# Kernel tuning notes

Measured on AMD Instinct MI355X. Metric: run time of the kernel, lower is better.

The kernel has to match this reference:

```python
import jax, jax.numpy as jnp
import numpy as np

B, C, N = 8, 64, 4096

def setup_inputs() -> dict:
    key = jax.random.key(0)
    k1, k2, k3 = jax.random.split(key, 3)
    k = jax.random.normal(k1, (B, C, N), dtype=jnp.float32)
    q = jax.random.normal(k2, (B, C, N), dtype=jnp.float32)
    v = jax.random.normal(k3, (B, C, N), dtype=jnpp.float32) if False else jax.random.normal(k3, (B, C, N), dtype=jnp.float32)
    return {"k": k, "q": q, "v": v}

def reference(k, q, v):
    input_dim = k.shape[1]  # C
    # similarity = k^T @ q : [B, N, N]
    scores = jnp.einsum('bcn,bcm->bnm', k, q) / jnp.sqrt(jnp.float32(input_dim))
    attn = jax.nn.softmax(scores, axis=-1)  # softmax over last dim (query positions m)
    # out = attn @ v^T : [B, N, C], then transpose back to [B, C, N]
    out = jnp.einsum('bnm,bcm->bcn', attn, v)
    return out
```

## Files before the change

kernel.cpp:

```cpp
#include <hip/hip_runtime.h>
#include <stdint.h>

typedef __attribute__((ext_vector_type(8)))  __bf16        bf16x8;
typedef __attribute__((ext_vector_type(8)))  unsigned short u16x8;
typedef __attribute__((ext_vector_type(4)))  float          f32x4;
typedef __attribute__((ext_vector_type(16))) float          f32x16;
typedef __attribute__((ext_vector_type(4)))  unsigned int   u32x4;

#define NB 8
#define NC 64
#define NN 4096
#define NCHUNK 64
#define CHUNK_U16 4096

#define EXP2F(x) __builtin_amdgcn_exp2f(x)

__device__ __forceinline__ unsigned short f2bf(float x) {
    unsigned int u = __builtin_bit_cast(unsigned int, x);
    u += 0x7fffu + ((u >> 16) & 1u);
    return (unsigned short)(u >> 16);
}
__device__ __forceinline__ unsigned int pk2(float a, float b) {
    unsigned short x = __builtin_bit_cast(unsigned short, (__bf16)a);
    unsigned short y = __builtin_bit_cast(unsigned short, (__bf16)b);
    return (unsigned int)x | ((unsigned int)y << 16);
}

__global__ __launch_bounds__(256) void prepass(
    const float* __restrict__ qp, const float* __restrict__ vp,
    unsigned short* __restrict__ qfo, unsigned short* __restrict__ vfo)
{
    __shared__ float lt[64][68];
    const int bid = blockIdx.x;
    const int b = bid >> 6, mc = bid & 63;
    const int m0 = mc * 64;
    const int tid = threadIdx.x;
    const float* qb = qp + (size_t)b * NC * NN;
    const float* vb = vp + (size_t)b * NC * NN;
    unsigned short* qfc = qfo + (size_t)bid * CHUNK_U16;
    unsigned short* vfc = vfo + (size_t)bid * CHUNK_U16;

    #pragma unroll
    for (int rep = 0; rep < 4; ++rep) {
        int idx = tid + 256 * rep;
        int c = idx >> 4, m4 = (idx & 15) << 2;
        f32x4 xv = *reinterpret_cast<const f32x4*>(qb + (size_t)c * NN + m0 + m4);
        lt[m4+0][c] = xv[0]; lt[m4+1][c] = xv[1];
        lt[m4+2][c] = xv[2]; lt[m4+3][c] = xv[3];
    }
    __syncthreads();
    #pragma unroll
    for (int rep = 0; rep < 2; ++rep) {
        int fid = tid + 256 * rep;
        int l = fid & 63, kk = (fid >> 6) & 3, mt = fid >> 8;
        int m = 32 * mt + (l & 31), c0 = 16 * kk + 8 * (l >> 5);
        u16x8 ov;
        #pragma unroll
        for (int e = 0; e < 8; ++e) ov[e] = f2bf(lt[m][c0 + e]);
        *reinterpret_cast<u16x8*>(qfc + (size_t)fid * 8) = ov;
    }
    __syncthreads();
    #pragma unroll
    for (int rep = 0; rep < 4; ++rep) {
        int idx = tid + 256 * rep;
        int c = idx >> 4, m4 = (idx & 15) << 2;
        f32x4 xv = *reinterpret_cast<const f32x4*>(vb + (size_t)c * NN + m0 + m4);
        *reinterpret_cast<f32x4*>(&lt[c][m4]) = xv;
    }
    __syncthreads();
    #pragma unroll
    for (int rep = 0; rep < 2; ++rep) {
        int fid = tid + 256 * rep;
        int l = fid & 63, kt = (fid >> 6) & 3, ct = fid >> 8;
        int c = 32 * ct + (l & 31), mm = 16 * kt + 8 * (l >> 5);
        u16x8 ov;
        #pragma unroll
        for (int e = 0; e < 8; ++e) ov[e] = f2bf(lt[c][mm + e]);
        *reinterpret_cast<u16x8*>(vfc + (size_t)fid * 8) = ov;
    }
}

template<int SPLITQ_T>
__global__ __launch_bounds__(128, 3) void attn4(
    const float* __restrict__ kp,
    const unsigned short* __restrict__ qfo,
    const unsigned short* __restrict__ vfo,
    float* __restrict__ part, float* __restrict__ lp)
{
    constexpr int CPQ_T = NCHUNK / SPLITQ_T;
    __shared__ unsigned short sq[2][CHUNK_U16];

    const int orig = blockIdx.x;
    constexpr int PER_XCD = 64 * SPLITQ_T;
    const int bid = (orig & 7) * PER_XCD + (orig >> 3);
    const int b = bid / PER_XCD;
    const int rest = bid % PER_XCD;
    const int tile = rest & 63;
    const int qid  = rest >> 6;
    const int n0 = tile * 64;
    const int tid = threadIdx.x;
    const int w = tid >> 6, l = tid & 63;
    const int lo5 = l & 31, hi = l >> 5;
    const int nrow = n0 + 32 * w + lo5;

    const float kscale = 0.125f * 1.44269504088896f;
    const float* kb = kp + (size_t)b * NC * NN;
    bf16x8 kf[4];
    #pragma unroll
    for (int kk = 0; kk < 4; ++kk) {
        u16x8 t;
        #pragma unroll
        for (int e = 0; e < 8; ++e)
            t[e] = __builtin_bit_cast(unsigned short,
                      (__bf16)(kscale * kb[(size_t)(16 * kk + 8 * hi + e) * NN + nrow]));
        kf[kk] = __builtin_bit_cast(bf16x8, t);
    }

    const unsigned short* qg = qfo + (size_t)(b * NCHUNK + qid * CPQ_T) * CHUNK_U16;
    const unsigned short* vg = vfo + (size_t)(b * NCHUNK + qid * CPQ_T) * CHUNK_U16;

    auto stage_q = [&](int mcr, int buf) {
        const unsigned short* gq = qg + (size_t)mcr * CHUNK_U16;
        #pragma unroll
        for (int i = 0; i < 4; ++i) {
            int seg = w * 4 + i;
            int off = seg * 512 + l * 8;
            __builtin_amdgcn_global_load_lds(
                (const __attribute__((address_space(1))) void*)(gq + off),
                (__attribute__((address_space(3))) void*)(&sq[buf][seg * 512]),
                16, 0, 0);
        }
    };

    stage_q(0, 0);
    __syncthreads();

    f32x16 o0, o1;
    #pragma unroll
    for (int r = 0; r < 16; ++r) { o0[r] = 0.f; o1[r] = 0.f; }
    float l_run = 0.f;

    for (int mcr = 0; mcr < CPQ_T; ++mcr) {
        const int cur = mcr & 1;
        u16x8 vf[8];
        #pragma unroll
        for (int f = 0; f < 8; ++f)
            vf[f] = *reinterpret_cast<const u16x8*>(vg + (size_t)mcr * CHUNK_U16 + (f * 64 + l) * 8);
        if (mcr + 1 < CPQ_T) stage_q(mcr + 1, cur ^ 1);
        const unsigned short* qb_ = &sq[cur][0];

        f32x16 s0, s1;
        #pragma unroll
        for (int r = 0; r < 16; ++r) { s0[r] = 0.f; s1[r] = 0.f; }
        #pragma unroll
        for (int kk = 0; kk < 4; ++kk) {
            u16x8 a0 = *reinterpret_cast<const u16x8*>(qb_ + ((0 * 4 + kk) * 64 + l) * 8);
            u16x8 a1 = *reinterpret_cast<const u16x8*>(qb_ + ((1 * 4 + kk) * 64 + l) * 8);
            s0 = __builtin_amdgcn_mfma_f32_32x32x16_bf16(__builtin_bit_cast(bf16x8, a0), kf[kk], s0, 0, 0, 0);
            s1 = __builtin_amdgcn_mfma_f32_32x32x16_bf16(__builtin_bit_cast(bf16x8, a1), kf[kk], s1, 0, 0, 0);
        }

        float sum = 0.f;
        #pragma unroll
        for (int r = 0; r < 16; ++r) { s0[r] = EXP2F(s0[r]); sum += s0[r]; }
        #pragma unroll
        for (int r = 0; r < 16; ++r) { s1[r] = EXP2F(s1[r]); sum += s1[r]; }
        sum += (float)__shfl_xor(sum, 32);
        l_run += sum;

        #pragma unroll
        for (int kt = 0; kt < 4; ++kt) {
            const f32x16& sm = (kt < 2) ? s0 : s1;
            const int qA = 2 * (kt & 1);
            unsigned int wA0 = pk2(sm[4 * qA + 0], sm[4 * qA + 1]);
            unsigned int wA1 = pk2(sm[4 * qA + 2], sm[4 * qA + 3]);
            unsigned int wB0 = pk2(sm[4 * qA + 4], sm[4 * qA + 5]);
            unsigned int wB1 = pk2(sm[4 * qA + 6], sm[4 * qA + 7]);
            unsigned int e0 = hi ? wA0 : wB0;
            unsigned int e1 = hi ? wA1 : wB1;
            e0 = (unsigned int)__shfl_xor((int)e0, 32);
            e1 = (unsigned int)__shfl_xor((int)e1, 32);
            u32x4 pf;
            if (hi == 0) pf = (u32x4){wA0, wA1, e0, e1};
            else         pf = (u32x4){e0, e1, wB0, wB1};
            bf16x8 pB = __builtin_bit_cast(bf16x8, pf);
            o0 = __builtin_amdgcn_mfma_f32_32x32x16_bf16(__builtin_bit_cast(bf16x8, vf[kt]),     pB, o0, 0, 0, 0);
            o1 = __builtin_amdgcn_mfma_f32_32x32x16_bf16(__builtin_bit_cast(bf16x8, vf[4 + kt]), pB, o1, 0, 0, 0);
        }
        __syncthreads();
    }

    const int pidx = (b * 64 + tile) * SPLITQ_T + qid;
    float* po = part + (size_t)pidx * 4096;
    const int rl = 32 * w + lo5;
    #pragma unroll
    for (int r = 0; r < 16; ++r) {
        int cb = (r & 3) + 8 * (r >> 2) + 4 * hi;
        po[cb * 64 + rl]        = o0[r];
        po[(32 + cb) * 64 + rl] = o1[r];
    }
    if (hi == 0) lp[(size_t)pidx * 64 + rl] = l_run;
}

__global__ __launch_bounds__(256) void combine2(
    const float* __restrict__ part, const float* __restrict__ lp,
    float* __restrict__ outp, int splitq)
{
    __shared__ float sinv[64];
    const int bid = blockIdx.x;
    const int b = bid >> 6, tile = bid & 63;
    const int n0 = tile * 64;
    const int t = threadIdx.x;
    const int pb = bid * splitq;

    if (t < 64) {
        float L = 0.f;
        for (int q = 0; q < splitq; ++q) L += lp[(size_t)(pb + q) * 64 + t];
        sinv[t] = 1.0f / L;
    }
    __syncthreads();

    float* ob = outp + (size_t)b * NC * NN;
    #pragma unroll
    for (int it = 0; it < 4; ++it) {
        int idx = it * 1024 + t * 4;
        int ch = idx >> 6, r0 = idx & 63;
        f32x4 acc = (f32x4){0.f, 0.f, 0.f, 0.f};
        for (int q = 0; q < splitq; ++q) {
            f32x4 v = *reinterpret_cast<const f32x4*>(part + (size_t)(pb + q) * 4096 + idx);
            acc += v;
        }
        f32x4 res;
        #pragma unroll
        for (int u = 0; u < 4; ++u) res[u] = acc[u] * sinv[r0 + u];
        *reinterpret_cast<f32x4*>(ob + (size_t)ch * NN + n0 + r0) = res;
    }
}

__global__ __launch_bounds__(128) void attn2(
    const float* __restrict__ kp,
    const unsigned short* __restrict__ qfo,
    const unsigned short* __restrict__ vfo,
    float* __restrict__ outp)
{
    __shared__ unsigned short sb[2][2 * CHUNK_U16];
    const int orig = blockIdx.x;
    const int bid  = (orig & 7) * 64 + (orig >> 3);
    const int b = bid >> 6, nt = bid & 63;
    const int n0 = nt * 64;
    const int tid = threadIdx.x;
    const int w = tid >> 6, l = tid & 63;
    const int lo5 = l & 31, hi = l >> 5;
    const int nrow = n0 + 32 * w + lo5;
    const float kscale = 0.125f * 1.44269504088896f;
    const float* kb = kp + (size_t)b * NC * NN;
    bf16x8 kf[4];
    #pragma unroll
    for (int kk = 0; kk < 4; ++kk) {
        u16x8 t;
        #pragma unroll
        for (int e = 0; e < 8; ++e)
            t[e] = f2bf(kscale * kb[(size_t)(16 * kk + 8 * hi + e) * NN + nrow]);
        kf[kk] = __builtin_bit_cast(bf16x8, t);
    }
    const unsigned short* qg = qfo + (size_t)(b * 64) * CHUNK_U16;
    const unsigned short* vg = vfo + (size_t)(b * 64) * CHUNK_U16;
    auto stage = [&](int mc, int buf) {
        const unsigned short* gq = qg + (size_t)mc * CHUNK_U16;
        const unsigned short* gv = vg + (size_t)mc * CHUNK_U16;
        #pragma unroll
        for (int i = 0; i < 4; ++i) {
            int seg = w * 4 + i;
            int off = seg * 512 + l * 8;
            __builtin_amdgcn_global_load_lds(
                (const __attribute__((address_space(1))) void*)(gq + off),
                (__attribute__((address_space(3))) void*)(&sb[buf][seg * 512]), 16, 0, 0);
            __builtin_amdgcn_global_load_lds(
                (const __attribute__((address_space(1))) void*)(gv + off),
                (__attribute__((address_space(3))) void*)(&sb[buf][CHUNK_U16 + seg * 512]), 16, 0, 0);
        }
    };
    stage(0, 0);
    __syncthreads();
    f32x16 o0, o1;
    #pragma unroll
    for (int r = 0; r < 16; ++r) { o0[r] = 0.f; o1[r] = 0.f; }
    float m_run = -1e30f, l_run = 0.f;
    for (int mc = 0; mc < NCHUNK; ++mc) {
        const int cur = mc & 1;
        if (mc + 1 < NCHUNK) stage(mc + 1, cur ^ 1);
        const unsigned short* qb_ = &sb[cur][0];
        const unsigned short* vb_ = &sb[cur][CHUNK_U16];
        f32x16 s0, s1;
        #pragma unroll
        for (int r = 0; r < 16; ++r) { s0[r] = 0.f; s1[r] = 0.f; }
        #pragma unroll
        for (int kk = 0; kk < 4; ++kk) {
            u16x8 a0 = *reinterpret_cast<const u16x8*>(qb_ + ((0 * 4 + kk) * 64 + l) * 8);
            u16x8 a1 = *reinterpret_cast<const u16x8*>(qb_ + ((1 * 4 + kk) * 64 + l) * 8);
            s0 = __builtin_amdgcn_mfma_f32_32x32x16_bf16(__builtin_bit_cast(bf16x8, a0), kf[kk], s0, 0, 0, 0);
            s1 = __builtin_amdgcn_mfma_f32_32x32x16_bf16(__builtin_bit_cast(bf16x8, a1), kf[kk], s1, 0, 0, 0);
        }
        float pmax = s0[0];
        #pragma unroll
        for (int r = 1; r < 16; ++r) pmax = fmaxf(pmax, s0[r]);
        #pragma unroll
        for (int r = 0; r < 16; ++r) pmax = fmaxf(pmax, s1[r]);
        pmax = fmaxf(pmax, (float)__shfl_xor(pmax, 32));
        const float mn = fmaxf(m_run, pmax);
        const float alpha = EXP2F(m_run - mn);
        float sum = 0.f;
        #pragma unroll
        for (int r = 0; r < 16; ++r) { s0[r] = EXP2F(s0[r] - mn); sum += s0[r]; }
        #pragma unroll
        for (int r = 0; r < 16; ++r) { s1[r] = EXP2F(s1[r] - mn); sum += s1[r]; }
        sum += (float)__shfl_xor(sum, 32);
        l_run = l_run * alpha + sum;
        m_run = mn;
        #pragma unroll
        for (int r = 0; r < 16; ++r) { o0[r] *= alpha; o1[r] *= alpha; }
        #pragma unroll
        for (int kt = 0; kt < 4; ++kt) {
            const f32x16& sm = (kt < 2) ? s0 : s1;
            const int qA = 2 * (kt & 1);
            unsigned int dA0 = pk2(sm[4 * qA + 0], sm[4 * qA + 1]);
            unsigned int dA1 = pk2(sm[4 * qA + 2], sm[4 * qA + 3]);
            unsigned int dB0 = pk2(sm[4 * qA + 4], sm[4 * qA + 5]);
            unsigned int dB1 = pk2(sm[4 * qA + 6], sm[4 * qA + 7]);
            unsigned int sA0 = (unsigned int)__shfl_xor((int)dA0, 32);
            unsigned int sA1 = (unsigned int)__shfl_xor((int)dA1, 32);
            unsigned int sB0 = (unsigned int)__shfl_xor((int)dB0, 32);
            unsigned int sB1 = (unsigned int)__shfl_xor((int)dB1, 32);
            u32x4 pf;
            if (hi == 0) pf = (u32x4){dA0, dA1, sA0, sA1};
            else         pf = (u32x4){sB0, sB1, dB0, dB1};
            bf16x8 pB = __builtin_bit_cast(bf16x8, pf);
            u16x8 v0 = *reinterpret_cast<const u16x8*>(vb_ + ((0 * 4 + kt) * 64 + l) * 8);
            u16x8 v1 = *reinterpret_cast<const u16x8*>(vb_ + ((1 * 4 + kt) * 64 + l) * 8);
            o0 = __builtin_amdgcn_mfma_f32_32x32x16_bf16(__builtin_bit_cast(bf16x8, v0), pB, o0, 0, 0, 0);
            o1 = __builtin_amdgcn_mfma_f32_32x32x16_bf16(__builtin_bit_cast(bf16x8, v1), pB, o1, 0, 0, 0);
        }
        __syncthreads();
    }
    const float inv = 1.0f / l_run;
    float* ob = outp + (size_t)b * NC * NN;
    #pragma unroll
    for (int r = 0; r < 16; ++r) {
        int cb = (r & 3) + 8 * (r >> 2) + 4 * hi;
        ob[(size_t)cb * NN + n0 + 32 * w + lo5]        = o0[r] * inv;
        ob[(size_t)(32 + cb) * NN + n0 + 32 * w + lo5] = o1[r] * inv;
    }
}

__global__ __launch_bounds__(256) void attn_fwd(
    const float* __restrict__ kp, const float* __restrict__ qp,
    const float* __restrict__ vp, float* __restrict__ outp)
{
    __shared__ unsigned short qs[8][64][8];
    __shared__ unsigned short vs[8][64][8];
    __shared__ unsigned short ps[4][2][64][8];
    const int orig = blockIdx.x;
    const int bid  = (orig & 7) * 64 + (orig >> 3);
    const int b  = bid >> 6;
    const int n0 = (bid & 63) * 64;
    const int tid = threadIdx.x;
    const int w = tid >> 6, l = tid & 63, g = l >> 4, j = l & 15;
    const float* kb = kp + (size_t)b * NC * NN;
    const float* qb = qp + (size_t)b * NC * NN;
    const float* vb = vp + (size_t)b * NC * NN;
    bf16x8 ak[2];
    #pragma unroll
    for (int kk = 0; kk < 2; ++kk) {
        u16x8 tmp;
        #pragma unroll
        for (int e = 0; e < 8; ++e)
            tmp[e] = f2bf(kb[(size_t)(32*kk + 8*g + e) * NN + (n0 + 16*w + j)]);
        ak[kk] = __builtin_bit_cast(bf16x8, tmp);
    }
    f32x4 o[4];
    float m_run[4], l_run[4];
    #pragma unroll
    for (int ct = 0; ct < 4; ++ct) o[ct] = (f32x4){0.f,0.f,0.f,0.f};
    #pragma unroll
    for (int r = 0; r < 4; ++r) { m_run[r] = -1e30f; l_run[r] = 0.0f; }
    for (int m0 = 0; m0 < NN; m0 += 64) {
        __syncthreads();
        #pragma unroll
        for (int it = 0; it < 4; ++it) {
            int f = tid + 256*it;
            int c = f >> 4, m4 = (f & 15) << 2;
            f32x4 qv = *reinterpret_cast<const f32x4*>(qb + (size_t)c*NN + m0 + m4);
            f32x4 vv = *reinterpret_cast<const f32x4*>(vb + (size_t)c*NN + m0 + m4);
            int kkq = c >> 5, eq = c & 7, gq = (c >> 3) & 3, tq = m4 >> 4;
            #pragma unroll
            for (int u = 0; u < 4; ++u)
                qs[kkq*4 + tq][16*gq + ((m4 + u) & 15)][eq] = f2bf(qv[u]);
            int ctv = c >> 4, jv = c & 15, kkv = m4 >> 5, gv = (m4 >> 3) & 3, ev = m4 & 7;
            #pragma unroll
            for (int u = 0; u < 4; ++u)
                vs[kkv*4 + ctv][16*gv + jv][ev + u] = f2bf(vv[u]);
        }
        __syncthreads();
        f32x4 s[4];
        #pragma unroll
        for (int t = 0; t < 4; ++t) {
            f32x4 acc = (f32x4){0.f,0.f,0.f,0.f};
            #pragma unroll
            for (int kk = 0; kk < 2; ++kk) {
                u16x8 raw = *reinterpret_cast<const u16x8*>(&qs[kk*4 + t][l][0]);
                acc = __builtin_amdgcn_mfma_f32_16x16x32_bf16(ak[kk], __builtin_bit_cast(bf16x8, raw), acc, 0,0,0);
            }
            s[t] = acc * 0.125f;
        }
        float alpha[4];
        #pragma unroll
        for (int r = 0; r < 4; ++r) {
            float m1 = fmaxf(fmaxf(s[0][r], s[1][r]), fmaxf(s[2][r], s[3][r]));
            #pragma unroll
            for (int off = 1; off < 16; off <<= 1) m1 = fmaxf(m1, __shfl_xor(m1, off));
            float mn = fmaxf(m_run[r], m1);
            alpha[r] = __expf(m_run[r] - mn);
            m_run[r] = mn;
            float acc = 0.0f;
            #pragma unroll
            for (int t = 0; t < 4; ++t) { float p = __expf(s[t][r] - mn); s[t][r] = p; acc += p; }
            #pragma unroll
            for (int off = 1; off < 16; off <<= 1) acc += __shfl_xor(acc, off);
            l_run[r] = l_run[r] * alpha[r] + acc;
        }
        {
            int srcl = (j >> 2) << 4;
            float a0 = __shfl(alpha[0], srcl), a1 = __shfl(alpha[1], srcl);
            float a2 = __shfl(alpha[2], srcl), a3 = __shfl(alpha[3], srcl);
            int rs = j & 3;
            float ac = (rs==0)?a0:(rs==1)?a1:(rs==2)?a2:a3;
            #pragma unroll
            for (int ct = 0; ct < 4; ++ct) o[ct] *= ac;
        }
        #pragma unroll
        for (int t = 0; t < 4; ++t) {
            int m = 16*t + j;
            #pragma unroll
            for (int r = 0; r < 4; ++r)
                ps[w][m >> 5][((m >> 3) & 3)*16 + 4*g + r][m & 7] = f2bf(s[t][r]);
        }
        asm volatile("s_waitcnt lgkmcnt(0)" ::: "memory");
        #pragma unroll
        for (int kk2 = 0; kk2 < 2; ++kk2) {
            u16x8 rp = *reinterpret_cast<const u16x8*>(&ps[w][kk2][l][0]);
            bf16x8 bp = __builtin_bit_cast(bf16x8, rp);
            #pragma unroll
            for (int ct = 0; ct < 4; ++ct) {
                u16x8 rv = *reinterpret_cast<const u16x8*>(&vs[kk2*4 + ct][l][0]);
                o[ct] = __builtin_amdgcn_mfma_f32_16x16x32_bf16(__builtin_bit_cast(bf16x8, rv), bp, o[ct], 0,0,0);
            }
        }
    }
    {
        int srcl = (j >> 2) << 4;
        float l0 = __shfl(l_run[0], srcl), l1 = __shfl(l_run[1], srcl);
        float l2 = __shfl(l_run[2], srcl), l3 = __shfl(l_run[3], srcl);
        int rs = j & 3;
        float lc = (rs==0)?l0:(rs==1)?l1:(rs==2)?l2:l3;
        float inv = 1.0f / lc;
        #pragma unroll
        for (int ct = 0; ct < 4; ++ct)
            #pragma unroll
            for (int r = 0; r < 4; ++r)
                outp[(size_t)b*NC*NN + (size_t)(16*ct + 4*g + r)*NN + (n0 + 16*w + j)] = o[ct][r] * inv;
    }
}

extern "C" void kernel_launch(void* const* d_in, const int* in_sizes, int n_in,
                              void* d_out, int out_size, void* d_ws, size_t ws_size,
                              hipStream_t stream) {
    const float* kp = (const float*)d_in[0];
    const float* qp = (const float*)d_in[1];
    const float* vp = (const float*)d_in[2];
    float* op = (float*)d_out;
    const size_t FRAG_BYTES = (size_t)2 * NB * NCHUNK * CHUNK_U16 * sizeof(unsigned short);
    unsigned short* qfo = (unsigned short*)d_ws;
    unsigned short* vfo = qfo + (size_t)NB * NCHUNK * CHUNK_U16;

    auto need = [&](int splitq) {
        return FRAG_BYTES
             + (size_t)NB * 64 * splitq * 4096 * sizeof(float)
             + (size_t)NB * 64 * splitq * 64 * sizeof(float);
    };

    int splitq = 0;
    if      (ws_size >= need(8)) splitq = 8;
    else if (ws_size >= need(4)) splitq = 4;

    if (splitq) {
        float* part = (float*)((char*)d_ws + FRAG_BYTES);
        float* lpp  = part + (size_t)NB * 64 * splitq * 4096;
        hipLaunchKernelGGL(prepass, dim3(NB * NCHUNK), dim3(256), 0, stream, qp, vp, qfo, vfo);
        if (splitq == 8)
            hipLaunchKernelGGL(attn4<8>, dim3(NB * 64 * 8), dim3(128), 0, stream, kp, qfo, vfo, part, lpp);
        else
            hipLaunchKernelGGL(attn4<4>, dim3(NB * 64 * 4), dim3(128), 0, stream, kp, qfo, vfo, part, lpp);
        hipLaunchKernelGGL(combine2, dim3(NB * 64), dim3(256), 0, stream, part, lpp, op, splitq);
    } else if (ws_size >= FRAG_BYTES) {
        hipLaunchKernelGGL(prepass, dim3(NB * NCHUNK), dim3(256), 0, stream, qp, vp, qfo, vfo);
        hipLaunchKernelGGL(attn2, dim3(NB * NCHUNK), dim3(128), 0, stream, kp, qfo, vfo, op);
    } else {
        hipLaunchKernelGGL(attn_fwd, dim3(512), dim3(256), 0, stream, kp, qp, vp, op);
    }
}
```

Before: 79.30 us.

## Replace two-wave attention blocks with single-wave blocks covering 64 rows each

```diff
diff --git a/kernel.cpp b/kernel.cpp
--- a/kernel.cpp
+++ b/kernel.cpp
@@ -12,6 +12,7 @@
 #define NN 4096
 #define NCHUNK 64
 #define CHUNK_U16 4096
+#define SPLITQ 4
 
 #define EXP2F(x) __builtin_amdgcn_exp2f(x)
 
@@ -81,125 +82,133 @@
 }
 
 template<int SPLITQ_T>
-__global__ __launch_bounds__(128, 3) void attn4(
+__global__ __launch_bounds__(64, 2) void attn5(
     const float* __restrict__ kp,
     const unsigned short* __restrict__ qfo,
     const unsigned short* __restrict__ vfo,
     float* __restrict__ part, float* __restrict__ lp)
 {
     constexpr int CPQ_T = NCHUNK / SPLITQ_T;
-    __shared__ unsigned short sq[2][CHUNK_U16];
-
+    constexpr int PER_XCD = 64 * SPLITQ_T;
     const int orig = blockIdx.x;
-    constexpr int PER_XCD = 64 * SPLITQ_T;
-    const int bid = (orig & 7) * PER_XCD + (orig >> 3);
-    const int b = bid / PER_XCD;
+    const int bid  = (orig & 7) * PER_XCD + (orig >> 3);
+    const int b    = bid / PER_XCD;
     const int rest = bid % PER_XCD;
+    const int qid  = rest >> 6;
     const int tile = rest & 63;
-    const int qid  = rest >> 6;
     const int n0 = tile * 64;
-    const int tid = threadIdx.x;
-    const int w = tid >> 6, l = tid & 63;
+    const int l = threadIdx.x;
     const int lo5 = l & 31, hi = l >> 5;
-    const int nrow = n0 + 32 * w + lo5;
 
     const float kscale = 0.125f * 1.44269504088896f;
     const float* kb = kp + (size_t)b * NC * NN;
-    bf16x8 kf[4];
+    bf16x8 kfA[4], kfB[4];
     #pragma unroll
     for (int kk = 0; kk < 4; ++kk) {
-        u16x8 t;
-        #pragma unroll
-        for (int e = 0; e < 8; ++e)
-            t[e] = __builtin_bit_cast(unsigned short,
-                      (__bf16)(kscale * kb[(size_t)(16 * kk + 8 * hi + e) * NN + nrow]));
-        kf[kk] = __builtin_bit_cast(bf16x8, t);
+        u16x8 tA, tB;
+        #pragma unroll
+        for (int e = 0; e < 8; ++e) {
+            size_t row = (size_t)(16 * kk + 8 * hi + e) * NN;
+            tA[e] = __builtin_bit_cast(unsigned short, (__bf16)(kscale * kb[row + n0 + lo5]));
+            tB[e] = __builtin_bit_cast(unsigned short, (__bf16)(kscale * kb[row + n0 + 32 + lo5]));
+        }
+        kfA[kk] = __builtin_bit_cast(bf16x8, tA);
+        kfB[kk] = __builtin_bit_cast(bf16x8, tB);
     }
 
     const unsigned short* qg = qfo + (size_t)(b * NCHUNK + qid * CPQ_T) * CHUNK_U16;
     const unsigned short* vg = vfo + (size_t)(b * NCHUNK + qid * CPQ_T) * CHUNK_U16;
 
-    auto stage_q = [&](int mcr, int buf) {
-        const unsigned short* gq = qg + (size_t)mcr * CHUNK_U16;
-        #pragma unroll
-        for (int i = 0; i < 4; ++i) {
-            int seg = w * 4 + i;
-            int off = seg * 512 + l * 8;
-            __builtin_amdgcn_global_load_lds(
-                (const __attribute__((address_space(1))) void*)(gq + off),
-                (__attribute__((address_space(3))) void*)(&sq[buf][seg * 512]),
-                16, 0, 0);
-        }
-    };
-
-    stage_q(0, 0);
-    __syncthreads();
-
-    f32x16 o0, o1;
-    #pragma unroll
-    for (int r = 0; r < 16; ++r) { o0[r] = 0.f; o1[r] = 0.f; }
-    float l_run = 0.f;
+    f32x16 zro;
+    #pragma unroll
+    for (int r = 0; r < 16; ++r) zro[r] = 0.f;
+    f32x16 oA0 = zro, oA1 = zro, oB0 = zro, oB1 = zro;
+    float sumA = 0.f, sumB = 0.f;
 
     for (int mcr = 0; mcr < CPQ_T; ++mcr) {
-        const int cur = mcr & 1;
+        const unsigned short* qc = qg + (size_t)mcr * CHUNK_U16;
+        const unsigned short* vc = vg + (size_t)mcr * CHUNK_U16;
+
+        u16x8 a[8];
+        #pragma unroll
+        for (int f = 0; f < 8; ++f)
+            a[f] = *reinterpret_cast<const u16x8*>(qc + (f * 64 + l) * 8);
+
+        f32x16 sA0 = __builtin_amdgcn_mfma_f32_32x32x16_bf16(__builtin_bit_cast(bf16x8, a[0]), kfA[0], zro, 0, 0, 0);
+        f32x16 sA1 = __builtin_amdgcn_mfma_f32_32x32x16_bf16(__builtin_bit_cast(bf16x8, a[4]), kfA[0], zro, 0, 0, 0);
+        f32x16 sB0 = __builtin_amdgcn_mfma_f32_32x32x16_bf16(__builtin_bit_cast(bf16x8, a[0]), kfB[0], zro, 0, 0, 0);
+        f32x16 sB1 = __builtin_amdgcn_mfma_f32_32x32x16_bf16(__builtin_bit_cast(bf16x8, a[4]), kfB[0], zro, 0, 0, 0);
+        #pragma unroll
+        for (int kk = 1; kk < 4; ++kk) {
+            bf16x8 a0 = __builtin_bit_cast(bf16x8, a[kk]);
+            bf16x8 a1 = __builtin_bit_cast(bf16x8, a[4 + kk]);
+            sA0 = __builtin_amdgcn_mfma_f32_32x32x16_bf16(a0, kfA[kk], sA0, 0, 0, 0);
+            sA1 = __builtin_amdgcn_mfma_f32_32x32x16_bf16(a1, kfA[kk], sA1, 0, 0, 0);
+            sB0 = __builtin_amdgcn_mfma_f32_32x32x16_bf16(a0, kfB[kk], sB0, 0, 0, 0);
+            sB1 = __builtin_amdgcn_mfma_f32_32x32x16_bf16(a1, kfB[kk], sB1, 0, 0, 0);
+        }
+
         u16x8 vf[8];
         #pragma unroll
         for (int f = 0; f < 8; ++f)
-            vf[f] = *reinterpret_cast<const u16x8*>(vg + (size_t)mcr * CHUNK_U16 + (f * 64 + l) * 8);
-        if (mcr + 1 < CPQ_T) stage_q(mcr + 1, cur ^ 1);
-        const unsigned short* qb_ = &sq[cur][0];
-
-        f32x16 s0, s1;
-        #pragma unroll
-        for (int r = 0; r < 16; ++r) { s0[r] = 0.f; s1[r] = 0.f; }
-        #pragma unroll
-        for (int kk = 0; kk < 4; ++kk) {
-            u16x8 a0 = *reinterpret_cast<const u16x8*>(qb_ + ((0 * 4 + kk) * 64 + l) * 8);
-            u16x8 a1 = *reinterpret_cast<const u16x8*>(qb_ + ((1 * 4 + kk) * 64 + l) * 8);
-            s0 = __builtin_amdgcn_mfma_f32_32x32x16_bf16(__builtin_bit_cast(bf16x8, a0), kf[kk], s0, 0, 0, 0);
-            s1 = __builtin_amdgcn_mfma_f32_32x32x16_bf16(__builtin_bit_cast(bf16x8, a1), kf[kk], s1, 0, 0, 0);
-        }
-
-        float sum = 0.f;
-        #pragma unroll
-        for (int r = 0; r < 16; ++r) { s0[r] = EXP2F(s0[r]); sum += s0[r]; }
-        #pragma unroll
-        for (int r = 0; r < 16; ++r) { s1[r] = EXP2F(s1[r]); sum += s1[r]; }
-        sum += (float)__shfl_xor(sum, 32);
-        l_run += sum;
+            vf[f] = *reinterpret_cast<const u16x8*>(vc + (f * 64 + l) * 8);
+
+        #pragma unroll
+        for (int r = 0; r < 16; ++r) { sA0[r] = EXP2F(sA0[r]); sumA += sA0[r]; }
+        #pragma unroll
+        for (int r = 0; r < 16; ++r) { sA1[r] = EXP2F(sA1[r]); sumA += sA1[r]; }
+        #pragma unroll
+        for (int r = 0; r < 16; ++r) { sB0[r] = EXP2F(sB0[r]); sumB += sB0[r]; }
+        #pragma unroll
+        for (int r = 0; r < 16; ++r) { sB1[r] = EXP2F(sB1[r]); sumB += sB1[r]; }
 
         #pragma unroll
         for (int kt = 0; kt < 4; ++kt) {
-            const f32x16& sm = (kt < 2) ? s0 : s1;
+            const f32x16& smA = (kt < 2) ? sA0 : sA1;
+            const f32x16& smB = (kt < 2) ? sB0 : sB1;
             const int qA = 2 * (kt & 1);
-            unsigned int wA0 = pk2(sm[4 * qA + 0], sm[4 * qA + 1]);
-            unsigned int wA1 = pk2(sm[4 * qA + 2], sm[4 * qA + 3]);
-            unsigned int wB0 = pk2(sm[4 * qA + 4], sm[4 * qA + 5]);
-            unsigned int wB1 = pk2(sm[4 * qA + 6], sm[4 * qA + 7]);
-            unsigned int e0 = hi ? wA0 : wB0;
-            unsigned int e1 = hi ? wA1 : wB1;
-            e0 = (unsigned int)__shfl_xor((int)e0, 32);
-            e1 = (unsigned int)__shfl_xor((int)e1, 32);
-            u32x4 pf;
-            if (hi == 0) pf = (u32x4){wA0, wA1, e0, e1};
-            else         pf = (u32x4){e0, e1, wB0, wB1};
-            bf16x8 pB = __builtin_bit_cast(bf16x8, pf);
-            o0 = __builtin_amdgcn_mfma_f32_32x32x16_bf16(__builtin_bit_cast(bf16x8, vf[kt]),     pB, o0, 0, 0, 0);
-            o1 = __builtin_amdgcn_mfma_f32_32x32x16_bf16(__builtin_bit_cast(bf16x8, vf[4 + kt]), pB, o1, 0, 0, 0);
-        }
-        __syncthreads();
-    }
-
+            unsigned int aw0 = pk2(smA[4*qA+0], smA[4*qA+1]);
+            unsigned int aw1 = pk2(smA[4*qA+2], smA[4*qA+3]);
+            unsigned int ax0 = pk2(smA[4*qA+4], smA[4*qA+5]);
+            unsigned int ax1 = pk2(smA[4*qA+6], smA[4*qA+7]);
+            unsigned int ae0 = (unsigned int)__shfl_xor((int)(hi ? aw0 : ax0), 32);
+            unsigned int ae1 = (unsigned int)__shfl_xor((int)(hi ? aw1 : ax1), 32);
+            u32x4 pfa = hi ? (u32x4){ae0, ae1, ax0, ax1} : (u32x4){aw0, aw1, ae0, ae1};
+            bf16x8 pBA = __builtin_bit_cast(bf16x8, pfa);
+            unsigned int bw0 = pk2(smB[4*qA+0], smB[4*qA+1]);
+            unsigned int bw1 = pk2(smB[4*qA+2], smB[4*qA+3]);
+            unsigned int bx0 = pk2(smB[4*qA+4], smB[4*qA+5]);
+            unsigned int bx1 = pk2(smB[4*qA+6], smB[4*qA+7]);
+            unsigned int be0 = (unsigned int)__shfl_xor((int)(hi ? bw0 : bx0), 32);
+            unsigned int be1 = (unsigned int)__shfl_xor((int)(hi ? bw1 : bx1), 32);
+            u32x4 pfb = hi ? (u32x4){be0, be1, bx0, bx1} : (u32x4){bw0, bw1, be0, be1};
+            bf16x8 pBB = __builtin_bit_cast(bf16x8, pfb);
+
+            bf16x8 v0 = __builtin_bit_cast(bf16x8, vf[kt]);
+            bf16x8 v1 = __builtin_bit_cast(bf16x8, vf[4 + kt]);
+            oA0 = __builtin_amdgcn_mfma_f32_32x32x16_bf16(v0, pBA, oA0, 0, 0, 0);
+            oA1 = __builtin_amdgcn_mfma_f32_32x32x16_bf16(v1, pBA, oA1, 0, 0, 0);
+            oB0 = __builtin_amdgcn_mfma_f32_32x32x16_bf16(v0, pBB, oB0, 0, 0, 0);
+            oB1 = __builtin_amdgcn_mfma_f32_32x32x16_bf16(v1, pBB, oB1, 0, 0, 0);
+        }
+    }
+
+    sumA += (float)__shfl_xor(sumA, 32);
+    sumB += (float)__shfl_xor(sumB, 32);
     const int pidx = (b * 64 + tile) * SPLITQ_T + qid;
     float* po = part + (size_t)pidx * 4096;
-    const int rl = 32 * w + lo5;
     #pragma unroll
     for (int r = 0; r < 16; ++r) {
         int cb = (r & 3) + 8 * (r >> 2) + 4 * hi;
-        po[cb * 64 + rl]        = o0[r];
-        po[(32 + cb) * 64 + rl] = o1[r];
-    }
-    if (hi == 0) lp[(size_t)pidx * 64 + rl] = l_run;
+        po[cb * 64 + lo5]             = oA0[r];
+        po[(32 + cb) * 64 + lo5]      = oA1[r];
+        po[cb * 64 + 32 + lo5]        = oB0[r];
+        po[(32 + cb) * 64 + 32 + lo5] = oB1[r];
+    }
+    if (hi == 0) {
+        lp[(size_t)pidx * 64 + lo5]      = sumA;
+        lp[(size_t)pidx * 64 + 32 + lo5] = sumB;
+    }
 }
 
 __global__ __launch_bounds__(256) void combine2(
@@ -482,25 +491,16 @@
     unsigned short* qfo = (unsigned short*)d_ws;
     unsigned short* vfo = qfo + (size_t)NB * NCHUNK * CHUNK_U16;
 
-    auto need = [&](int splitq) {
-        return FRAG_BYTES
-             + (size_t)NB * 64 * splitq * 4096 * sizeof(float)
-             + (size_t)NB * 64 * splitq * 64 * sizeof(float);
-    };
-
-    int splitq = 0;
-    if      (ws_size >= need(8)) splitq = 8;
-    else if (ws_size >= need(4)) splitq = 4;
-
-    if (splitq) {
+    const size_t NEED = FRAG_BYTES
+        + (size_t)NB * 64 * SPLITQ * 4096 * sizeof(float)
+        + (size_t)NB * 64 * SPLITQ * 64 * sizeof(float);
+
+    if (ws_size >= NEED) {
         float* part = (float*)((char*)d_ws + FRAG_BYTES);
-        float* lpp  = part + (size_t)NB * 64 * splitq * 4096;
+        float* lpp  = part + (size_t)NB * 64 * SPLITQ * 4096;
         hipLaunchKernelGGL(prepass, dim3(NB * NCHUNK), dim3(256), 0, stream, qp, vp, qfo, vfo);
-        if (splitq == 8)
-            hipLaunchKernelGGL(attn4<8>, dim3(NB * 64 * 8), dim3(128), 0, stream, kp, qfo, vfo, part, lpp);
-        else
-            hipLaunchKernelGGL(attn4<4>, dim3(NB * 64 * 4), dim3(128), 0, stream, kp, qfo, vfo, part, lpp);
-        hipLaunchKernelGGL(combine2, dim3(NB * 64), dim3(256), 0, stream, part, lpp, op, splitq);
+        hipLaunchKernelGGL(attn5<SPLITQ>, dim3(NB * 64 * SPLITQ), dim3(64), 0, stream, kp, qfo, vfo, part, lpp);
+        hipLaunchKernelGGL(combine2, dim3(NB * 64), dim3(256), 0, stream, part, lpp, op, SPLITQ);
     } else if (ws_size >= FRAG_BYTES) {
         hipLaunchKernelGGL(prepass, dim3(NB * NCHUNK), dim3(256), 0, stream, qp, vp, qfo, vfo);
         hipLaunchKernelGGL(attn2, dim3(NB * NCHUNK), dim3(128), 0, stream, kp, qfo, vfo, op);
```

New measurement: 66.72 us. -15.9%, faster.

## Widen attention blocks to 128 rows and stage V through LDS

Applied to the files above, without the earlier changes.

```diff
diff --git a/kernel.cpp b/kernel.cpp
--- a/kernel.cpp
+++ b/kernel.cpp
@@ -12,6 +12,7 @@
 #define NN 4096
 #define NCHUNK 64
 #define CHUNK_U16 4096
+#define SPLITQ 4
 
 #define EXP2F(x) __builtin_amdgcn_exp2f(x)
 
@@ -31,7 +32,8 @@
     unsigned short* __restrict__ qfo, unsigned short* __restrict__ vfo)
 {
     __shared__ float lt[64][68];
-    const int bid = blockIdx.x;
+    const int orig = blockIdx.x;
+    const int bid = (orig & 7) * 64 + (orig >> 3);
     const int b = bid >> 6, mc = bid & 63;
     const int m0 = mc * 64;
     const int tid = threadIdx.x;
@@ -81,27 +83,28 @@
 }
 
 template<int SPLITQ_T>
-__global__ __launch_bounds__(128, 3) void attn4(
+__global__ __launch_bounds__(256, 3) void attn7(
     const float* __restrict__ kp,
     const unsigned short* __restrict__ qfo,
     const unsigned short* __restrict__ vfo,
     float* __restrict__ part, float* __restrict__ lp)
 {
     constexpr int CPQ_T = NCHUNK / SPLITQ_T;
-    __shared__ unsigned short sq[2][CHUNK_U16];
+    constexpr int TG = NN / 128;
+    constexpr int PER_XCD = SPLITQ_T * TG;
+    __shared__ unsigned short sb[2][2 * CHUNK_U16];
 
     const int orig = blockIdx.x;
-    constexpr int PER_XCD = 64 * SPLITQ_T;
-    const int bid = (orig & 7) * PER_XCD + (orig >> 3);
-    const int b = bid / PER_XCD;
+    const int bid  = (orig & 7) * PER_XCD + (orig >> 3);
+    const int b    = bid / PER_XCD;
     const int rest = bid % PER_XCD;
-    const int tile = rest & 63;
-    const int qid  = rest >> 6;
-    const int n0 = tile * 64;
+    const int qid  = rest / TG;
+    const int tg   = rest % TG;
+    const int bn0  = tg * 128;
     const int tid = threadIdx.x;
     const int w = tid >> 6, l = tid & 63;
     const int lo5 = l & 31, hi = l >> 5;
-    const int nrow = n0 + 32 * w + lo5;
+    const int nrow = bn0 + 32 * w + lo5;
 
     const float kscale = 0.125f * 1.44269504088896f;
     const float* kb = kp + (size_t)b * NC * NN;
@@ -119,87 +122,90 @@
     const unsigned short* qg = qfo + (size_t)(b * NCHUNK + qid * CPQ_T) * CHUNK_U16;
     const unsigned short* vg = vfo + (size_t)(b * NCHUNK + qid * CPQ_T) * CHUNK_U16;
 
-    auto stage_q = [&](int mcr, int buf) {
+    auto stage = [&](int mcr, int buf) {
         const unsigned short* gq = qg + (size_t)mcr * CHUNK_U16;
-        #pragma unroll
-        for (int i = 0; i < 4; ++i) {
-            int seg = w * 4 + i;
-            int off = seg * 512 + l * 8;
+        const unsigned short* gv = vg + (size_t)mcr * CHUNK_U16;
+        #pragma unroll
+        for (int j = 0; j < 2; ++j) {
+            int off = w * 1024 + j * 512 + l * 8;
             __builtin_amdgcn_global_load_lds(
                 (const __attribute__((address_space(1))) void*)(gq + off),
-                (__attribute__((address_space(3))) void*)(&sq[buf][seg * 512]),
+                (__attribute__((address_space(3))) void*)(&sb[buf][w * 1024 + j * 512]),
                 16, 0, 0);
+            __builtin_amdgcn_global_load_lds(
+                (const __attribute__((address_space(1))) void*)(gv + off),
+                (__attribute__((address_space(3))) void*)(&sb[buf][CHUNK_U16 + w * 1024 + j * 512]),
+                16, 0, 0);
         }
     };
 
-    stage_q(0, 0);
+    stage(0, 0);
     __syncthreads();
 
-    f32x16 o0, o1;
-    #pragma unroll
-    for (int r = 0; r < 16; ++r) { o0[r] = 0.f; o1[r] = 0.f; }
-    float l_run = 0.f;
+    f32x16 zro;
+    #pragma unroll
+    for (int r = 0; r < 16; ++r) zro[r] = 0.f;
+    f32x16 o0 = zro, o1 = zro;
+    float sum = 0.f;
 
     for (int mcr = 0; mcr < CPQ_T; ++mcr) {
         const int cur = mcr & 1;
-        u16x8 vf[8];
+        if (mcr + 1 < CPQ_T) stage(mcr + 1, cur ^ 1);
+        const unsigned short* qb_ = &sb[cur][0];
+        const unsigned short* vb_ = &sb[cur][CHUNK_U16];
+
+        u16x8 a[8];
         #pragma unroll
         for (int f = 0; f < 8; ++f)
-            vf[f] = *reinterpret_cast<const u16x8*>(vg + (size_t)mcr * CHUNK_U16 + (f * 64 + l) * 8);
-        if (mcr + 1 < CPQ_T) stage_q(mcr + 1, cur ^ 1);
-        const unsigned short* qb_ = &sq[cur][0];
-
-        f32x16 s0, s1;
-        #pragma unroll
-        for (int r = 0; r < 16; ++r) { s0[r] = 0.f; s1[r] = 0.f; }
-        #pragma unroll
-        for (int kk = 0; kk < 4; ++kk) {
-            u16x8 a0 = *reinterpret_cast<const u16x8*>(qb_ + ((0 * 4 + kk) * 64 + l) * 8);
-            u16x8 a1 = *reinterpret_cast<const u16x8*>(qb_ + ((1 * 4 + kk) * 64 + l) * 8);
-            s0 = __builtin_amdgcn_mfma_f32_32x32x16_bf16(__builtin_bit_cast(bf16x8, a0), kf[kk], s0, 0, 0, 0);
-            s1 = __builtin_amdgcn_mfma_f32_32x32x16_bf16(__builtin_bit_cast(bf16x8, a1), kf[kk], s1, 0, 0, 0);
-        }
-
-        float sum = 0.f;
+            a[f] = *reinterpret_cast<const u16x8*>(qb_ + (f * 64 + l) * 8);
+
+        f32x16 s0 = __builtin_amdgcn_mfma_f32_32x32x16_bf16(__builtin_bit_cast(bf16x8, a[0]), kf[0], zro, 0, 0, 0);
+        f32x16 s1 = __builtin_amdgcn_mfma_f32_32x32x16_bf16(__builtin_bit_cast(bf16x8, a[4]), kf[0], zro, 0, 0, 0);
+        #pragma unroll
+        for (int kk = 1; kk < 4; ++kk) {
+            s0 = __builtin_amdgcn_mfma_f32_32x32x16_bf16(__builtin_bit_cast(bf16x8, a[kk]),     kf[kk], s0, 0, 0, 0);
+            s1 = __builtin_amdgcn_mfma_f32_32x32x16_bf16(__builtin_bit_cast(bf16x8, a[4 + kk]), kf[kk], s1, 0, 0, 0);
+        }
+
+        #pragma unroll
+        for (int f = 0; f < 8; ++f)
+            a[f] = *reinterpret_cast<const u16x8*>(vb_ + (f * 64 + l) * 8);
+
         #pragma unroll
         for (int r = 0; r < 16; ++r) { s0[r] = EXP2F(s0[r]); sum += s0[r]; }
         #pragma unroll
         for (int r = 0; r < 16; ++r) { s1[r] = EXP2F(s1[r]); sum += s1[r]; }
-        sum += (float)__shfl_xor(sum, 32);
-        l_run += sum;
 
         #pragma unroll
         for (int kt = 0; kt < 4; ++kt) {
             const f32x16& sm = (kt < 2) ? s0 : s1;
             const int qA = 2 * (kt & 1);
-            unsigned int wA0 = pk2(sm[4 * qA + 0], sm[4 * qA + 1]);
-            unsigned int wA1 = pk2(sm[4 * qA + 2], sm[4 * qA + 3]);
-            unsigned int wB0 = pk2(sm[4 * qA + 4], sm[4 * qA + 5]);
-            unsigned int wB1 = pk2(sm[4 * qA + 6], sm[4 * qA + 7]);
-            unsigned int e0 = hi ? wA0 : wB0;
-            unsigned int e1 = hi ? wA1 : wB1;
-            e0 = (unsigned int)__shfl_xor((int)e0, 32);
-            e1 = (unsigned int)__shfl_xor((int)e1, 32);
-            u32x4 pf;
-            if (hi == 0) pf = (u32x4){wA0, wA1, e0, e1};
-            else         pf = (u32x4){e0, e1, wB0, wB1};
+            unsigned int wA0 = pk2(sm[4*qA+0], sm[4*qA+1]);
+            unsigned int wA1 = pk2(sm[4*qA+2], sm[4*qA+3]);
+            unsigned int wB0 = pk2(sm[4*qA+4], sm[4*qA+5]);
+            unsigned int wB1 = pk2(sm[4*qA+6], sm[4*qA+7]);
+            unsigned int e0 = (unsigned int)__shfl_xor((int)(hi ? wA0 : wB0), 32);
+            unsigned int e1 = (unsigned int)__shfl_xor((int)(hi ? wA1 : wB1), 32);
+            u32x4 pf = hi ? (u32x4){e0, e1, wB0, wB1} : (u32x4){wA0, wA1, e0, e1};
             bf16x8 pB = __builtin_bit_cast(bf16x8, pf);
-            o0 = __builtin_amdgcn_mfma_f32_32x32x16_bf16(__builtin_bit_cast(bf16x8, vf[kt]),     pB, o0, 0, 0, 0);
-            o1 = __builtin_amdgcn_mfma_f32_32x32x16_bf16(__builtin_bit_cast(bf16x8, vf[4 + kt]), pB, o1, 0, 0, 0);
+            o0 = __builtin_amdgcn_mfma_f32_32x32x16_bf16(__builtin_bit_cast(bf16x8, a[kt]),     pB, o0, 0, 0, 0);
+            o1 = __builtin_amdgcn_mfma_f32_32x32x16_bf16(__builtin_bit_cast(bf16x8, a[4 + kt]), pB, o1, 0, 0, 0);
         }
         __syncthreads();
     }
 
-    const int pidx = (b * 64 + tile) * SPLITQ_T + qid;
+    sum += (float)__shfl_xor(sum, 32);
+    const int t64 = (bn0 >> 6) + (w >> 1);
+    const int rowoff = 32 * (w & 1);
+    const int pidx = (b * 64 + t64) * SPLITQ_T + qid;
     float* po = part + (size_t)pidx * 4096;
-    const int rl = 32 * w + lo5;
     #pragma unroll
     for (int r = 0; r < 16; ++r) {
         int cb = (r & 3) + 8 * (r >> 2) + 4 * hi;
-        po[cb * 64 + rl]        = o0[r];
-        po[(32 + cb) * 64 + rl] = o1[r];
-    }
-    if (hi == 0) lp[(size_t)pidx * 64 + rl] = l_run;
+        po[cb * 64 + rowoff + lo5]        = o0[r];
+        po[(32 + cb) * 64 + rowoff + lo5] = o1[r];
+    }
+    if (hi == 0) lp[(size_t)pidx * 64 + rowoff + lo5] = sum;
 }
 
 __global__ __launch_bounds__(256) void combine2(
@@ -207,7 +213,8 @@
     float* __restrict__ outp, int splitq)
 {
     __shared__ float sinv[64];
-    const int bid = blockIdx.x;
+    const int orig = blockIdx.x;
+    const int bid = (orig & 7) * 64 + (orig >> 3);
     const int b = bid >> 6, tile = bid & 63;
     const int n0 = tile * 64;
     const int t = threadIdx.x;
@@ -482,25 +489,17 @@
     unsigned short* qfo = (unsigned short*)d_ws;
     unsigned short* vfo = qfo + (size_t)NB * NCHUNK * CHUNK_U16;
 
-    auto need = [&](int splitq) {
-        return FRAG_BYTES
-             + (size_t)NB * 64 * splitq * 4096 * sizeof(float)
-             + (size_t)NB * 64 * splitq * 64 * sizeof(float);
-    };
-
-    int splitq = 0;
-    if      (ws_size >= need(8)) splitq = 8;
-    else if (ws_size >= need(4)) splitq = 4;
-
-    if (splitq) {
+    const size_t NEED = FRAG_BYTES
+        + (size_t)NB * 64 * SPLITQ * 4096 * sizeof(float)
+        + (size_t)NB * 64 * SPLITQ * 64 * sizeof(float);
+
+    if (ws_size >= NEED) {
         float* part = (float*)((char*)d_ws + FRAG_BYTES);
-        float* lpp  = part + (size_t)NB * 64 * splitq * 4096;
+        float* lpp  = part + (size_t)NB * 64 * SPLITQ * 4096;
         hipLaunchKernelGGL(prepass, dim3(NB * NCHUNK), dim3(256), 0, stream, qp, vp, qfo, vfo);
-        if (splitq == 8)
-            hipLaunchKernelGGL(attn4<8>, dim3(NB * 64 * 8), dim3(128), 0, stream, kp, qfo, vfo, part, lpp);
-        else
-            hipLaunchKernelGGL(attn4<4>, dim3(NB * 64 * 4), dim3(128), 0, stream, kp, qfo, vfo, part, lpp);
-        hipLaunchKernelGGL(combine2, dim3(NB * 64), dim3(256), 0, stream, part, lpp, op, splitq);
+        hipLaunchKernelGGL(attn7<SPLITQ>, dim3(NB * SPLITQ * (NN / 128)), dim3(256), 0, stream,
+                           kp, qfo, vfo, part, lpp);
+        hipLaunchKernelGGL(combine2, dim3(NB * 64), dim3(256), 0, stream, part, lpp, op, SPLITQ);
     } else if (ws_size >= FRAG_BYTES) {
         hipLaunchKernelGGL(prepass, dim3(NB * NCHUNK), dim3(256), 0, stream, qp, vp, qfo, vfo);
         hipLaunchKernelGGL(attn2, dim3(NB * NCHUNK), dim3(128), 0, stream, kp, qfo, vfo, op);
```

Result: faster. 68.87 us (-13.1%).
